# Kernel tuning notes

Hardware: AMD Instinct MI355X
Metric: run time of the kernel (lower is better)

## Reference

```python
import jax, jax.numpy as jnp
import numpy as np

B, N, D_IN, HID = 8, 2048, 256, 64  # batch, nodes, input hidden, graph hidden (heads=1)
NEG_INF = -9e15  # matches -9000000000000000.0 in the torch code


def setup_inputs() -> dict:
    key = jax.random.key(0)
    k1, k2, k3, k4 = jax.random.split(key, 4)
    node_features = jax.random.normal(k1, (B, N, D_IN), dtype=jnp.float32)
    adj = jax.random.randint(k2, (B, N, N), 0, 2, dtype=jnp.int32)
    W = jax.random.normal(k3, (D_IN, HID), dtype=jnp.float32) / np.sqrt(D_IN).astype(np.float32)
    a = jax.random.normal(k4, (2 * HID, 1), dtype=jnp.float32) * 0.1
    return {"node_features": node_features, "adj": adj, "W": W, "a": a}


def reference(node_features, adj, W, a):
    # Wh = W(node_features): (B, N, HID)
    Wh = jnp.einsum('bnd,dh->bnh', node_features, W)
    a1 = a[:HID, 0]   # attention vector for the 'source' half of the concat
    a2 = a[HID:, 0]   # attention vector for the 'neighbor' half
    f1 = Wh @ a1      # (B, N) = Wh_i . a1
    f2 = Wh @ a2      # (B, N) = Wh_j . a2
    # e_ij = leakyrelu([Wh_i || Wh_j] . a) -- avoids the O(N^2 * 2*HID) concat
    e = jax.nn.leaky_relu(f1[:, :, None] + f2[:, None, :], negative_slope=0.2)  # (B, N, N)
    att = jnp.where(adj > 0, e, jnp.float32(NEG_INF))
    att = jax.nn.softmax(att, axis=2)
    # dropout is identity in eval / with graph_dropout=0.0
    h_prime = jnp.einsum('bij,bjh->bih', att, Wh)  # (B, N, HID)
    return h_prime
```

## Files before the change

kernel.cpp:

```cpp
#include <hip/hip_runtime.h>

#define NB 8
#define NN 2048
#define DIN 256
#define HID 64
#define JSPLIT 8

typedef _Float16 f16x8_t __attribute__((ext_vector_type(8)));
typedef _Float16 f16x2_t __attribute__((ext_vector_type(2)));
typedef _Float16 f16x4_t __attribute__((ext_vector_type(4)));
typedef float f32x16_t __attribute__((ext_vector_type(16)));

__global__ __launch_bounds__(256) void k_prep(
    const float* __restrict__ x, const float* __restrict__ W,
    const float* __restrict__ a, const int* __restrict__ adj,
    unsigned long long* __restrict__ mb, _Float16* __restrict__ wht,
    float* __restrict__ f1, float* __restrict__ f2)
{
    __shared__ float smem[DIN * 64];
    const int bid = blockIdx.x;
    const int t = threadIdx.x;

    if (bid >= 256) {
        const int lane = t & 63;
        const int wave = (bid - 256) * 4 + (t >> 6);
#pragma unroll
        for (int rr = 0; rr < 2; ++rr) {
            const int row = wave * 2 + rr;
            const int* ar = adj + (size_t)row * NN;
            unsigned long long myw = 0;
#pragma unroll
            for (int k = 0; k < 32; ++k) {
                unsigned long long bal = __ballot(ar[k * 64 + lane] != 0);
                if ((lane & 31) == k) myw = bal;
            }
            if (lane < 32) mb[(size_t)row * 32 + lane] = myw;
        }
        return;
    }

    const int g0 = bid * 64;
    const int b = g0 >> 11;
    const int n0 = g0 & (NN - 1);

    const float4* x4 = (const float4*)x;
#pragma unroll
    for (int it = 0; it < 16; ++it) {
        int c = t + it * 256;
        int row = c & 63;
        int dg = c >> 6;
        float4 v = x4[(size_t)(g0 + row) * 64 + dg];
        smem[(dg * 4 + 0) * 64 + row] = v.x;
        smem[(dg * 4 + 1) * 64 + row] = v.y;
        smem[(dg * 4 + 2) * 64 + row] = v.z;
        smem[(dg * 4 + 3) * 64 + row] = v.w;
    }
    __syncthreads();

    const int hq = t & 15;
    const int rg = t >> 4;
    const float4* W4 = (const float4*)W;
    float acc[4][4] = {};
#pragma unroll 8
    for (int d = 0; d < DIN; ++d) {
        float4 wv = W4[d * 16 + hq];
        float4 xv = *(const float4*)&smem[d * 64 + rg * 4];
        float xr[4] = {xv.x, xv.y, xv.z, xv.w};
        float wk[4] = {wv.x, wv.y, wv.z, wv.w};
#pragma unroll
        for (int r = 0; r < 4; ++r)
#pragma unroll
            for (int k = 0; k < 4; ++k) acc[r][k] += xr[r] * wk[k];
    }

    float4 a1v = ((const float4*)a)[hq];
    float4 a2v = ((const float4*)a)[16 + hq];
#pragma unroll
    for (int r = 0; r < 4; ++r) {
        float p1 = acc[r][0] * a1v.x + acc[r][1] * a1v.y + acc[r][2] * a1v.z + acc[r][3] * a1v.w;
        float p2 = acc[r][0] * a2v.x + acc[r][1] * a2v.y + acc[r][2] * a2v.z + acc[r][3] * a2v.w;
#pragma unroll
        for (int m = 1; m < 16; m <<= 1) {
            p1 += __shfl_xor(p1, m);
            p2 += __shfl_xor(p2, m);
        }
        if (hq == 0) {
            f1[g0 + rg * 4 + r] = p1;
            f2[g0 + rg * 4 + r] = p2;
        }
    }

    __syncthreads();
#pragma unroll
    for (int r = 0; r < 4; ++r)
#pragma unroll
        for (int k = 0; k < 4; ++k) {
            int h = hq * 4 + k;
            int row = rg * 4 + r;
            smem[h * 64 + (((row >> 2) ^ (h & 15)) << 2) + (row & 3)] = acc[r][k];
        }
    __syncthreads();

    const int h = t >> 2;
    const int rc = t & 3;
    union { _Float16 fh[16]; uint4 u4[2]; } uh;
#pragma unroll
    for (int q = 0; q < 4; ++q) {
        float4 v = *(const float4*)&smem[h * 64 + (((rc * 4 + q) ^ (h & 15)) << 2)];
        uh.fh[q * 4 + 0] = (_Float16)v.x;
        uh.fh[q * 4 + 1] = (_Float16)v.y;
        uh.fh[q * 4 + 2] = (_Float16)v.z;
        uh.fh[q * 4 + 3] = (_Float16)v.w;
    }
    size_t obase = (size_t)(b * HID + h) * NN + n0 + rc * 16;
    *(uint4*)&wht[obase] = uh.u4[0];
    *(uint4*)&wht[obase + 8] = uh.u4[1];
}

__global__ __launch_bounds__(256) void k_f2max(
    const float* __restrict__ f2, float* __restrict__ f2mx)
{
    __shared__ float red[4];
    const int b = blockIdx.x, t = threadIdx.x;
    float m = -3.4e38f;
    for (int i = t; i < NN; i += 256) m = fmaxf(m, f2[b * NN + i]);
#pragma unroll
    for (int s = 1; s < 64; s <<= 1) m = fmaxf(m, __shfl_xor(m, s));
    if ((t & 63) == 0) red[t >> 6] = m;
    __syncthreads();
    if (t == 0) f2mx[b] = fmaxf(fmaxf(red[0], red[1]), fmaxf(red[2], red[3]));
}

__global__ __launch_bounds__(256, 4) void k_attn(
    const unsigned long long* __restrict__ mb, const _Float16* __restrict__ wht,
    const float* __restrict__ f1, const float* __restrict__ f2,
    const float* __restrict__ f2mx,
    _Float16* __restrict__ accp, float* __restrict__ zp)
{
    __shared__ _Float16 whx[64 * 128];
    const int t = threadIdx.x;
    const int w = t >> 6, lane = t & 63;
    const int bx = blockIdx.x;
    const int js = bx & 7;
    const int it = (bx >> 3) & 15;
    const int b = bx >> 7;
    const int I0 = it * 128 + w * 32;
    const int half = lane >> 5;
    const int m32 = lane & 31;
    const int row = I0 + m32;
    const int jb0 = js * 256;

    const float f1v = f1[b * NN + row];
    float Mi = f1v + f2mx[b];
    Mi = Mi > 0.f ? Mi : 0.2f * Mi;
    const float LOG2E = 1.4426950408889634f;
    const float negMiL = -Mi * LOG2E;
    const float* f2p = f2 + b * NN;

    const unsigned long long* mrow = mb + (size_t)(b * NN + row) * 32 + js * 4;
    unsigned long long m[4];
    {
        ulonglong2 q0 = *(const ulonglong2*)mrow;
        ulonglong2 q1 = *(const ulonglong2*)(mrow + 2);
        m[0] = q0.x; m[1] = q0.y; m[2] = q1.x; m[3] = q1.y;
    }

    f16x8_t bones;
#pragma unroll
    for (int i = 0; i < 8; ++i) bones[i] = (_Float16)1.0f;

    f32x16_t acc0, acc1, acc2;
#pragma unroll
    for (int i = 0; i < 16; ++i) { acc0[i] = 0.f; acc1[i] = 0.f; acc2[i] = 0.f; }

#pragma unroll
    for (int stg = 0; stg < 2; ++stg) {
        const int jt = jb0 + stg * 128;
        if (stg) __syncthreads();
#pragma unroll
        for (int cc = 0; cc < 4; ++cc) {
            int c = t + cc * 256;
            int h = c >> 4, g = c & 15;
            int gp = g ^ (h & 15);
            size_t src = (size_t)(b * HID + h) * NN + jt + g * 8;
            *(uint4*)&whx[h * 128 + gp * 8] = *(const uint4*)&wht[src];
        }
        __syncthreads();
#pragma unroll
        for (int s8 = 0; s8 < 8; ++s8) {
            const int jl = jt + s8 * 16 + half * 8;
            const uint32_t bits8 =
                (uint32_t)(m[stg * 2 + (s8 >> 2)] >> (((s8 & 3) * 16) + half * 8)) & 0xffu;
            float4 fa = *(const float4*)&f2p[jl];
            float4 fb = *(const float4*)&f2p[jl + 4];
            float fv[8] = {fa.x, fa.y, fa.z, fa.w, fb.x, fb.y, fb.z, fb.w};
            union { f16x2_t h2[4]; f16x8_t v; } ua;
#pragma unroll
            for (int jp = 0; jp < 4; ++jp) {
                float pv[2];
#pragma unroll
                for (int e = 0; e < 2; ++e) {
                    int jj = jp * 2 + e;
                    float t1 = f1v + fv[jj];
                    t1 = fmaxf(t1, 0.2f * t1);
                    pv[e] = (bits8 & (1u << jj))
                          ? __builtin_amdgcn_exp2f(fmaf(t1, LOG2E, negMiL))
                          : 0.f;
                }
                auto pk = __builtin_amdgcn_cvt_pkrtz(pv[0], pv[1]);
                ua.h2[jp] = *(f16x2_t*)&pk;
            }
            const int gx = (2 * s8 + half) ^ (m32 & 15);
            f16x8_t b0 = *(const f16x8_t*)&whx[m32 * 128 + (gx << 3)];
            f16x8_t b1 = *(const f16x8_t*)&whx[(m32 + 32) * 128 + (gx << 3)];
            acc0 = __builtin_amdgcn_mfma_f32_32x32x16_f16(ua.v, b0, acc0, 0, 0, 0);
            acc1 = __builtin_amdgcn_mfma_f32_32x32x16_f16(ua.v, b1, acc1, 0, 0, 0);
            acc2 = __builtin_amdgcn_mfma_f32_32x32x16_f16(ua.v, bones, acc2, 0, 0, 0);
        }
    }

    float* zb = zp + (size_t)(js * NB + b) * NN;
    _Float16* ap = accp + (size_t)(js * NB + b) * NN * HID;
#pragma unroll
    for (int r = 0; r < 16; ++r) {
        int rr = (r & 3) + 8 * (r >> 2) + 4 * half;
        if (m32 == 0) zb[I0 + rr] = acc2[r];
        ap[(size_t)(I0 + rr) * HID + m32] = (_Float16)acc0[r];
        ap[(size_t)(I0 + rr) * HID + m32 + 32] = (_Float16)acc1[r];
    }
}

__global__ __launch_bounds__(256) void k_combine(
    const _Float16* __restrict__ accp, const float* __restrict__ zp,
    float* __restrict__ out)
{
    int gid = blockIdx.x * 256 + threadIdx.x;
    int h4 = gid & 15;
    int rowg = gid >> 4;
    float z = 0.f;
    float s0 = 0.f, s1 = 0.f, s2 = 0.f, s3 = 0.f;
#pragma unroll
    for (int js = 0; js < JSPLIT; ++js) {
        size_t base = (size_t)js * NB * NN;
        z += zp[base + rowg];
        f16x4_t v = *(const f16x4_t*)&accp[(base + rowg) * HID + h4 * 4];
        s0 += (float)v[0]; s1 += (float)v[1]; s2 += (float)v[2]; s3 += (float)v[3];
    }
    float zi = 1.f / z;
    float4 o = {s0 * zi, s1 * zi, s2 * zi, s3 * zi};
    ((float4*)out)[gid] = o;
}

extern "C" void kernel_launch(void* const* d_in, const int* in_sizes, int n_in,
                              void* d_out, int out_size, void* d_ws, size_t ws_size,
                              hipStream_t stream)
{
    const float* x = (const float*)d_in[0];
    const int* adj = (const int*)d_in[1];
    const float* W = (const float*)d_in[2];
    const float* a = (const float*)d_in[3];
    float* out = (float*)d_out;
    char* ws = (char*)d_ws;

    _Float16* wht = (_Float16*)(ws);
    float* f1   = (float*)(ws + (2u << 20));
    float* f2   = (float*)(ws + (2u << 20) + (64u << 10));
    float* f2mx = (float*)(ws + (2u << 20) + (128u << 10));
    unsigned long long* mbuf = (unsigned long long*)(ws + (3u << 20));
    _Float16* accp = (_Float16*)(ws + (8u << 20));
    float* zp   = (float*)(ws + (24u << 20));

    hipLaunchKernelGGL(k_prep, dim3(2304), dim3(256), 0, stream,
                       x, W, a, adj, mbuf, wht, f1, f2);
    hipLaunchKernelGGL(k_f2max, dim3(NB), dim3(256), 0, stream, f2, f2mx);
    hipLaunchKernelGGL(k_attn, dim3(1024), dim3(256), 0, stream, mbuf, wht, f1, f2, f2mx, accp, zp);
    hipLaunchKernelGGL(k_combine, dim3(1024), dim3(256), 0, stream, accp, zp, out);
}
```

Measured before the change: 226.9 us.

## Read int adjacency directly in attention kernel instead of building bitmask

Removes the bitmask-packing stage from the prep kernel and has the attention kernel load the int32 adjacency rows directly, with a one-step software prefetch of the next 8 entries. The aim is to avoid writing and then re-reading a packed mask and to shrink the prep launch. In exchange, the attention kernel now streams the full 128 MB int32 adjacency itself with strided per-lane loads, which may add memory stalls to the MFMA loop and raise register pressure.

Measured after the change: 243.2 us. 7.2% more time.

```diff
diff --git a/kernel.cpp b/kernel.cpp
--- a/kernel.cpp
+++ b/kernel.cpp
@@ -13,31 +13,12 @@
 
 __global__ __launch_bounds__(256) void k_prep(
     const float* __restrict__ x, const float* __restrict__ W,
-    const float* __restrict__ a, const int* __restrict__ adj,
-    unsigned long long* __restrict__ mb, _Float16* __restrict__ wht,
+    const float* __restrict__ a, _Float16* __restrict__ wht,
     float* __restrict__ f1, float* __restrict__ f2)
 {
     __shared__ float smem[DIN * 64];
     const int bid = blockIdx.x;
     const int t = threadIdx.x;
-
-    if (bid >= 256) {
-        const int lane = t & 63;
-        const int wave = (bid - 256) * 4 + (t >> 6);
-#pragma unroll
-        for (int rr = 0; rr < 2; ++rr) {
-            const int row = wave * 2 + rr;
-            const int* ar = adj + (size_t)row * NN;
-            unsigned long long myw = 0;
-#pragma unroll
-            for (int k = 0; k < 32; ++k) {
-                unsigned long long bal = __ballot(ar[k * 64 + lane] != 0);
-                if ((lane & 31) == k) myw = bal;
-            }
-            if (lane < 32) mb[(size_t)row * 32 + lane] = myw;
-        }
-        return;
-    }
 
     const int g0 = bid * 64;
     const int b = g0 >> 11;
@@ -132,7 +113,7 @@
 }
 
 __global__ __launch_bounds__(256, 4) void k_attn(
-    const unsigned long long* __restrict__ mb, const _Float16* __restrict__ wht,
+    const int* __restrict__ adj, const _Float16* __restrict__ wht,
     const float* __restrict__ f1, const float* __restrict__ f2,
     const float* __restrict__ f2mx,
     _Float16* __restrict__ accp, float* __restrict__ zp)
@@ -157,13 +138,11 @@
     const float negMiL = -Mi * LOG2E;
     const float* f2p = f2 + b * NN;
 
-    const unsigned long long* mrow = mb + (size_t)(b * NN + row) * 32 + js * 4;
-    unsigned long long m[4];
-    {
-        ulonglong2 q0 = *(const ulonglong2*)mrow;
-        ulonglong2 q1 = *(const ulonglong2*)(mrow + 2);
-        m[0] = q0.x; m[1] = q0.y; m[2] = q1.x; m[3] = q1.y;
-    }
+    const int4* ar4 = (const int4*)(adj + (size_t)(b * NN + row) * NN);
+    const int base4 = (jb0 >> 2) + half * 2;
+    int cur = base4;
+    int4 c0 = ar4[cur];
+    int4 c1 = ar4[cur + 1];
 
     f16x8_t bones;
 #pragma unroll
@@ -188,12 +167,16 @@
         __syncthreads();
 #pragma unroll
         for (int s8 = 0; s8 < 8; ++s8) {
+            const bool lastit = (stg == 1) && (s8 == 7);
+            const int nxt = lastit ? base4 : (cur + 4);
+            int4 n0 = ar4[nxt];
+            int4 n1 = ar4[nxt + 1];
+
             const int jl = jt + s8 * 16 + half * 8;
-            const uint32_t bits8 =
-                (uint32_t)(m[stg * 2 + (s8 >> 2)] >> (((s8 & 3) * 16) + half * 8)) & 0xffu;
             float4 fa = *(const float4*)&f2p[jl];
             float4 fb = *(const float4*)&f2p[jl + 4];
             float fv[8] = {fa.x, fa.y, fa.z, fa.w, fb.x, fb.y, fb.z, fb.w};
+            int av[8] = {c0.x, c0.y, c0.z, c0.w, c1.x, c1.y, c1.z, c1.w};
             union { f16x2_t h2[4]; f16x8_t v; } ua;
 #pragma unroll
             for (int jp = 0; jp < 4; ++jp) {
@@ -203,7 +186,7 @@
                     int jj = jp * 2 + e;
                     float t1 = f1v + fv[jj];
                     t1 = fmaxf(t1, 0.2f * t1);
-                    pv[e] = (bits8 & (1u << jj))
+                    pv[e] = av[jj]
                           ? __builtin_amdgcn_exp2f(fmaf(t1, LOG2E, negMiL))
                           : 0.f;
                 }
@@ -216,6 +199,8 @@
             acc0 = __builtin_amdgcn_mfma_f32_32x32x16_f16(ua.v, b0, acc0, 0, 0, 0);
             acc1 = __builtin_amdgcn_mfma_f32_32x32x16_f16(ua.v, b1, acc1, 0, 0, 0);
             acc2 = __builtin_amdgcn_mfma_f32_32x32x16_f16(ua.v, bones, acc2, 0, 0, 0);
+
+            c0 = n0; c1 = n1; cur = nxt;
         }
     }
 
@@ -266,13 +251,12 @@
     float* f1   = (float*)(ws + (2u << 20));
     float* f2   = (float*)(ws + (2u << 20) + (64u << 10));
     float* f2mx = (float*)(ws + (2u << 20) + (128u << 10));
-    unsigned long long* mbuf = (unsigned long long*)(ws + (3u << 20));
     _Float16* accp = (_Float16*)(ws + (8u << 20));
     float* zp   = (float*)(ws + (24u << 20));
 
-    hipLaunchKernelGGL(k_prep, dim3(2304), dim3(256), 0, stream,
-                       x, W, a, adj, mbuf, wht, f1, f2);
+    hipLaunchKernelGGL(k_prep, dim3(256), dim3(256), 0, stream,
+                       x, W, a, wht, f1, f2);
     hipLaunchKernelGGL(k_f2max, dim3(NB), dim3(256), 0, stream, f2, f2mx);
-    hipLaunchKernelGGL(k_attn, dim3(1024), dim3(256), 0, stream, mbuf, wht, f1, f2, f2mx, accp, zp);
+    hipLaunchKernelGGL(k_attn, dim3(1024), dim3(256), 0, stream, adj, wht, f1, f2, f2mx, accp, zp);
     hipLaunchKernelGGL(k_combine, dim3(1024), dim3(256), 0, stream, accp, zp, out);
 }
```

## Fuse split-J combine into attention kernel via in-block LDS reduction

Applied to the files above, without the earlier changes.

Restructures k_attn so each block owns 32 rows and its four waves split the J dimension (512 columns each), then reduces the partial accumulators and row sums through LDS and writes the normalized output directly. This removes the k_combine launch and the fp16 partial-accumulator round trip through global memory. In exchange the grid halves to 512 blocks, LDS use grows to 64 KB per block, and the occupancy hint is dropped, which may lower occupancy and latency hiding.

New measurement: 231.4 us. 1.02x slower.

```diff
diff --git a/kernel.cpp b/kernel.cpp
--- a/kernel.cpp
+++ b/kernel.cpp
@@ -4,11 +4,9 @@
 #define NN 2048
 #define DIN 256
 #define HID 64
-#define JSPLIT 8
 
 typedef _Float16 f16x8_t __attribute__((ext_vector_type(8)));
 typedef _Float16 f16x2_t __attribute__((ext_vector_type(2)));
-typedef _Float16 f16x4_t __attribute__((ext_vector_type(4)));
 typedef float f32x16_t __attribute__((ext_vector_type(16)));
 
 __global__ __launch_bounds__(256) void k_prep(
@@ -131,24 +129,23 @@
     if (t == 0) f2mx[b] = fmaxf(fmaxf(red[0], red[1]), fmaxf(red[2], red[3]));
 }
 
-__global__ __launch_bounds__(256, 4) void k_attn(
+__global__ __launch_bounds__(256) void k_attn(
     const unsigned long long* __restrict__ mb, const _Float16* __restrict__ wht,
     const float* __restrict__ f1, const float* __restrict__ f2,
     const float* __restrict__ f2mx,
-    _Float16* __restrict__ accp, float* __restrict__ zp)
-{
-    __shared__ _Float16 whx[64 * 128];
+    float* __restrict__ out)
+{
+    __shared__ _Float16 whx[4 * 64 * 128];
     const int t = threadIdx.x;
     const int w = t >> 6, lane = t & 63;
     const int bx = blockIdx.x;
-    const int js = bx & 7;
-    const int it = (bx >> 3) & 15;
-    const int b = bx >> 7;
-    const int I0 = it * 128 + w * 32;
+    const int it = bx & 63;
+    const int b = bx >> 6;
+    const int I0 = it * 32;
     const int half = lane >> 5;
     const int m32 = lane & 31;
     const int row = I0 + m32;
-    const int jb0 = js * 256;
+    const int jq0 = w * 512;
 
     const float f1v = f1[b * NN + row];
     float Mi = f1v + f2mx[b];
@@ -157,12 +154,12 @@
     const float negMiL = -Mi * LOG2E;
     const float* f2p = f2 + b * NN;
 
-    const unsigned long long* mrow = mb + (size_t)(b * NN + row) * 32 + js * 4;
-    unsigned long long m[4];
-    {
-        ulonglong2 q0 = *(const ulonglong2*)mrow;
-        ulonglong2 q1 = *(const ulonglong2*)(mrow + 2);
-        m[0] = q0.x; m[1] = q0.y; m[2] = q1.x; m[3] = q1.y;
+    const unsigned long long* mrow = mb + (size_t)(b * NN + row) * 32 + w * 8;
+    unsigned long long m[8];
+#pragma unroll
+    for (int q = 0; q < 4; ++q) {
+        ulonglong2 qq = *(const ulonglong2*)(mrow + q * 2);
+        m[q * 2] = qq.x; m[q * 2 + 1] = qq.y;
     }
 
     f16x8_t bones;
@@ -173,24 +170,24 @@
 #pragma unroll
     for (int i = 0; i < 16; ++i) { acc0[i] = 0.f; acc1[i] = 0.f; acc2[i] = 0.f; }
 
-#pragma unroll
-    for (int stg = 0; stg < 2; ++stg) {
-        const int jt = jb0 + stg * 128;
-        if (stg) __syncthreads();
-#pragma unroll
-        for (int cc = 0; cc < 4; ++cc) {
-            int c = t + cc * 256;
-            int h = c >> 4, g = c & 15;
+    for (int s = 0; s < 4; ++s) {
+        if (s) __syncthreads();
+#pragma unroll
+        for (int cc = 0; cc < 16; ++cc) {
+            int id = t + cc * 256;
+            int g = id & 15;
+            int h = (id >> 4) & 63;
+            int slab = id >> 10;
             int gp = g ^ (h & 15);
-            size_t src = (size_t)(b * HID + h) * NN + jt + g * 8;
-            *(uint4*)&whx[h * 128 + gp * 8] = *(const uint4*)&wht[src];
+            size_t src = (size_t)(b * HID + h) * NN + slab * 512 + s * 128 + g * 8;
+            *(uint4*)&whx[slab * 8192 + h * 128 + gp * 8] = *(const uint4*)&wht[src];
         }
         __syncthreads();
 #pragma unroll
         for (int s8 = 0; s8 < 8; ++s8) {
-            const int jl = jt + s8 * 16 + half * 8;
+            const int jl = jq0 + s * 128 + s8 * 16 + half * 8;
             const uint32_t bits8 =
-                (uint32_t)(m[stg * 2 + (s8 >> 2)] >> (((s8 & 3) * 16) + half * 8)) & 0xffu;
+                (uint32_t)(m[s * 2 + (s8 >> 2)] >> (((s8 & 3) * 16) + half * 8)) & 0xffu;
             float4 fa = *(const float4*)&f2p[jl];
             float4 fb = *(const float4*)&f2p[jl + 4];
             float fv[8] = {fa.x, fa.y, fa.z, fa.w, fb.x, fb.y, fb.z, fb.w};
@@ -211,44 +208,44 @@
                 ua.h2[jp] = *(f16x2_t*)&pk;
             }
             const int gx = (2 * s8 + half) ^ (m32 & 15);
-            f16x8_t b0 = *(const f16x8_t*)&whx[m32 * 128 + (gx << 3)];
-            f16x8_t b1 = *(const f16x8_t*)&whx[(m32 + 32) * 128 + (gx << 3)];
+            f16x8_t b0 = *(const f16x8_t*)&whx[w * 8192 + m32 * 128 + (gx << 3)];
+            f16x8_t b1 = *(const f16x8_t*)&whx[w * 8192 + (m32 + 32) * 128 + (gx << 3)];
             acc0 = __builtin_amdgcn_mfma_f32_32x32x16_f16(ua.v, b0, acc0, 0, 0, 0);
             acc1 = __builtin_amdgcn_mfma_f32_32x32x16_f16(ua.v, b1, acc1, 0, 0, 0);
             acc2 = __builtin_amdgcn_mfma_f32_32x32x16_f16(ua.v, bones, acc2, 0, 0, 0);
         }
     }
 
-    float* zb = zp + (size_t)(js * NB + b) * NN;
-    _Float16* ap = accp + (size_t)(js * NB + b) * NN * HID;
+    __syncthreads();
+    float* F = (float*)whx;
+    float* Z = (float*)whx + 4 * 32 * 64;
 #pragma unroll
     for (int r = 0; r < 16; ++r) {
         int rr = (r & 3) + 8 * (r >> 2) + 4 * half;
-        if (m32 == 0) zb[I0 + rr] = acc2[r];
-        ap[(size_t)(I0 + rr) * HID + m32] = (_Float16)acc0[r];
-        ap[(size_t)(I0 + rr) * HID + m32 + 32] = (_Float16)acc1[r];
-    }
-}
-
-__global__ __launch_bounds__(256) void k_combine(
-    const _Float16* __restrict__ accp, const float* __restrict__ zp,
-    float* __restrict__ out)
-{
-    int gid = blockIdx.x * 256 + threadIdx.x;
-    int h4 = gid & 15;
-    int rowg = gid >> 4;
+        F[(w * 32 + rr) * 64 + m32] = acc0[r];
+        F[(w * 32 + rr) * 64 + m32 + 32] = acc1[r];
+        if (m32 == 0) Z[w * 32 + rr] = acc2[r];
+    }
+    __syncthreads();
+
+    const int orow = t >> 3;
+    const int oc = (t & 7) * 8;
+    float4 s0 = {0.f, 0.f, 0.f, 0.f}, s1 = {0.f, 0.f, 0.f, 0.f};
     float z = 0.f;
-    float s0 = 0.f, s1 = 0.f, s2 = 0.f, s3 = 0.f;
-#pragma unroll
-    for (int js = 0; js < JSPLIT; ++js) {
-        size_t base = (size_t)js * NB * NN;
-        z += zp[base + rowg];
-        f16x4_t v = *(const f16x4_t*)&accp[(base + rowg) * HID + h4 * 4];
-        s0 += (float)v[0]; s1 += (float)v[1]; s2 += (float)v[2]; s3 += (float)v[3];
+#pragma unroll
+    for (int ww = 0; ww < 4; ++ww) {
+        z += Z[ww * 32 + orow];
+        float4 u0 = *(const float4*)&F[(ww * 32 + orow) * 64 + oc];
+        float4 u1 = *(const float4*)&F[(ww * 32 + orow) * 64 + oc + 4];
+        s0.x += u0.x; s0.y += u0.y; s0.z += u0.z; s0.w += u0.w;
+        s1.x += u1.x; s1.y += u1.y; s1.z += u1.z; s1.w += u1.w;
     }
     float zi = 1.f / z;
-    float4 o = {s0 * zi, s1 * zi, s2 * zi, s3 * zi};
-    ((float4*)out)[gid] = o;
+    s0.x *= zi; s0.y *= zi; s0.z *= zi; s0.w *= zi;
+    s1.x *= zi; s1.y *= zi; s1.z *= zi; s1.w *= zi;
+    float* op = out + (size_t)(b * NN + I0 + orow) * HID + oc;
+    *(float4*)op = s0;
+    *(float4*)(op + 4) = s1;
 }
 
 extern "C" void kernel_launch(void* const* d_in, const int* in_sizes, int n_in,
@@ -267,12 +264,10 @@
     float* f2   = (float*)(ws + (2u << 20) + (64u << 10));
     float* f2mx = (float*)(ws + (2u << 20) + (128u << 10));
     unsigned long long* mbuf = (unsigned long long*)(ws + (3u << 20));
-    _Float16* accp = (_Float16*)(ws + (8u << 20));
-    float* zp   = (float*)(ws + (24u << 20));
 
     hipLaunchKernelGGL(k_prep, dim3(2304), dim3(256), 0, stream,
                        x, W, a, adj, mbuf, wht, f1, f2);
     hipLaunchKernelGGL(k_f2max, dim3(NB), dim3(256), 0, stream, f2, f2mx);
-    hipLaunchKernelGGL(k_attn, dim3(1024), dim3(256), 0, stream, mbuf, wht, f1, f2, f2mx, accp, zp);
-    hipLaunchKernelGGL(k_combine, dim3(1024), dim3(256), 0, stream, accp, zp, out);
-}
+    hipLaunchKernelGGL(k_attn, dim3(512), dim3(256), 0, stream,
+                       mbuf, wht, f1, f2, f2mx, out);
+}
```
